# Kernel tuning notes

Hardware: AMD Instinct MI355X
Metric: run time of the kernel (lower is better)

## Reference

```python
import jax, jax.numpy as jnp
import numpy as np

EPS = 1e-6

def setup_inputs() -> dict:
    key = jax.random.key(0)
    ks = jax.random.split(key, 8)
    I, S, O = 1024, 512, 1024
    Bsz, T = 4, 2048
    return {
        "u": jax.random.normal(ks[0], (Bsz, T, I), dtype=jnp.float32),
        "dt": jax.random.normal(ks[1], (S,), dtype=jnp.float32),
        "A": jax.random.normal(ks[2], (S,), dtype=jnp.float32),
        "Bmat": jax.random.normal(ks[3], (I, S), dtype=jnp.float32) / np.sqrt(S),
        "C": jax.random.normal(ks[4], (S, O), dtype=jnp.float32) / np.sqrt(S),
        "D": jax.random.normal(ks[5], (O,), dtype=jnp.float32),
        "norm_w": jnp.ones((I,), dtype=jnp.float32),
    }

def _rmsnorm(x, w):
    x32 = x.astype(jnp.float32)
    n = x32 * jax.lax.rsqrt(jnp.mean(x32 * x32, axis=-1, keepdims=True) + EPS)
    return n.astype(x.dtype) * w

def reference(u, dt, A, Bmat, C, D, norm_w):
    u = _rmsnorm(u, norm_w)                      # [B, T, I]
    Bsz, T, _ = u.shape
    dts = jax.nn.sigmoid(dt)                     # [S]
    a = jnp.exp(-dts * jnp.abs(A))               # [S] discretized decay
    t = jnp.arange(T, dtype=jnp.float32)
    h = dts[:, None] * a[:, None] ** t[None, :]  # [S, T] geometric kernel
    u_proj = jnp.einsum('bti,is->bst', u, Bmat)  # [B, S, T]
    # depthwise causal conv: flipped kernel + cross-correlation == convolution
    k = jnp.flip(h, axis=1)[:, None, :]          # [S, 1, T] (OIW)
    x = jax.lax.conv_general_dilated(
        u_proj, k, window_strides=(1,), padding=[(T - 1, T - 1)],
        dimension_numbers=('NCW', 'OIW', 'NCW'),
        feature_group_count=u_proj.shape[1])[:, :, :T]  # [B, S, T]
    x = jnp.transpose(x, (0, 2, 1))              # [B, T, S]
    y = jnp.einsum('bts,so->bto', x, C) + D      # [B, T, O]
    return (y, x[:, -1])
```

## Files before the change

### kernel.cpp

```cpp
#include <hip/hip_runtime.h>
#include <math.h>

#define I_DIM 1024
#define S_DIM 512
#define O_DIM 1024
#define T_DIM 2048
#define B_SZ 4
#define M_ROWS (B_SZ * T_DIM)
#define EPSF 1e-6f

#define CL 64
#define NCH 32

typedef _Float16 f16;
typedef __attribute__((ext_vector_type(8))) _Float16 f16x8;
typedef __attribute__((ext_vector_type(2))) _Float16 f16x2;
typedef __attribute__((ext_vector_type(4))) float f32x4;

__device__ __forceinline__ unsigned short f2h_bits(float f) {
    _Float16 h = (_Float16)f;
    return __builtin_bit_cast(unsigned short, h);
}

__device__ __forceinline__ void load16_lds(const void* g, void* l) {
    __builtin_amdgcn_global_load_lds((const __attribute__((address_space(1))) void*)g,
                                     (__attribute__((address_space(3))) void*)l,
                                     16, 0, 0);
}

__global__ __launch_bounds__(256)
void prep_w(const float* __restrict__ Bmat, const float* __restrict__ dt,
            const float* __restrict__ nw, unsigned short* __restrict__ Bt16,
            const float* __restrict__ Cmat, unsigned short* __restrict__ Ct16) {
    __shared__ float tile[32][33];
    const int t = threadIdx.x;
    const int tx = t & 31, ty = t >> 5;
    const int bx = blockIdx.x;
    if (bx < 512) {
        const int bs = (bx & 15) * 32;
        const int bi = (bx >> 4) * 32;
        #pragma unroll
        for (int i = ty; i < 32; i += 8)
            tile[i][tx] = Bmat[(size_t)(bi + i) * S_DIM + bs + tx];
        __syncthreads();
        const float w = nw[bi + tx];
        #pragma unroll
        for (int i = ty; i < 32; i += 8) {
            const int s = bs + i;
            const float dts = 1.0f / (1.0f + expf(-dt[s]));
            Bt16[(size_t)s * I_DIM + bi + tx] = f2h_bits(tile[tx][i] * dts * w);
        }
    } else {
        const int tb = bx - 512;
        const int bo = (tb & 31) * 32;
        const int bs = (tb >> 5) * 32;
        #pragma unroll
        for (int i = ty; i < 32; i += 8)
            tile[i][tx] = Cmat[(size_t)(bs + i) * O_DIM + bo + tx];
        __syncthreads();
        #pragma unroll
        for (int i = ty; i < 32; i += 8)
            Ct16[(size_t)(bo + i) * S_DIM + bs + tx] = f2h_bits(tile[tx][i]);
    }
}

__global__ __launch_bounds__(256)
void gemm1_rms_chfin(const float* __restrict__ U, const f16* __restrict__ Bt,
                     f16* __restrict__ up, float* __restrict__ chlast,
                     const float* __restrict__ dt, const float* __restrict__ Avec) {
    constexpr int K = I_DIM, N = S_DIM, NK = K / 32;
    __shared__ f16 As[3][64 * 32];
    __shared__ f16 Bs[3][128 * 32];
    __shared__ float rsbuf[64];
    const int t = threadIdx.x;

    int bid = blockIdx.x;
    bid = (bid & 7) * 64 + (bid >> 3);
    const int n0 = (bid & 3) * 128;
    const int m0 = (bid >> 2) * 64;
    const int wid = t >> 6, lane = t & 63;
    const int wn = wid * 32, lr = lane & 15, kg = lane >> 4;

    const int swch = (t & 3) ^ ((t >> 3) & 3);
    const float* aptr = U + (size_t)(m0 + (t >> 2)) * K + swch * 8;
    const f16*  bptr = Bt + (size_t)(n0 + (t >> 2)) * K + swch * 8;
    const int rchunk = (kg ^ ((lr >> 1) & 3)) * 8;
    f16* adst = (f16*)&As[0][0] + t * 8;

    float ss = 0.f;
    f32x4 acc[4][2];
    #pragma unroll
    for (int i = 0; i < 4; ++i)
        #pragma unroll
        for (int j = 0; j < 2; ++j) acc[i][j] = (f32x4){0.f, 0.f, 0.f, 0.f};

    float4 rga[2], rgb[2];

    auto stageB = [&](int kt, int slot) {
        load16_lds(bptr + kt * 32, &Bs[slot][t * 8]);
        load16_lds(bptr + (size_t)64 * K + kt * 32, &Bs[slot][2048 + t * 8]);
    };
    auto writeA = [&](const float4* r, int slot) {
        ss += r[0].x * r[0].x + r[0].y * r[0].y + r[0].z * r[0].z + r[0].w * r[0].w
            + r[1].x * r[1].x + r[1].y * r[1].y + r[1].z * r[1].z + r[1].w * r[1].w;
        f16x8 h = { (_Float16)r[0].x, (_Float16)r[0].y, (_Float16)r[0].z, (_Float16)r[0].w,
                    (_Float16)r[1].x, (_Float16)r[1].y, (_Float16)r[1].z, (_Float16)r[1].w };
        *(f16x8*)(adst + slot * 2048) = h;
    };

    rga[0] = *(const float4*)(aptr);
    rga[1] = *(const float4*)(aptr + 4);
    stageB(0, 0);
    rgb[0] = *(const float4*)(aptr + 32);
    rgb[1] = *(const float4*)(aptr + 36);
    stageB(1, 1);
    asm volatile("s_waitcnt vmcnt(6)");
    writeA(rga, 0);

    #pragma unroll 2
    for (int kt = 0; kt < NK; ++kt) {
        asm volatile("s_waitcnt lgkmcnt(0)");
        if (kt + 1 < NK) asm volatile("s_waitcnt vmcnt(2)");
        else             asm volatile("s_waitcnt vmcnt(0)");
        __builtin_amdgcn_s_barrier();
        __builtin_amdgcn_sched_barrier(0);

        if (kt + 1 < NK)
            writeA(((kt + 1) & 1) ? rgb : rga, (kt + 1) % 3);
        if (kt + 2 < NK) {
            float4* r = (kt & 1) ? rgb : rga;
            const int k2 = (kt + 2) * 32;
            r[0] = *(const float4*)(aptr + k2);
            r[1] = *(const float4*)(aptr + k2 + 4);
            stageB(kt + 2, (kt + 2) % 3);
        }

        const int slot = kt % 3;
        f16x8 af[4], bf[2];
        #pragma unroll
        for (int m = 0; m < 4; ++m)
            af[m] = *(const f16x8*)&As[slot][(m * 16 + lr) * 32 + rchunk];
        #pragma unroll
        for (int n = 0; n < 2; ++n)
            bf[n] = *(const f16x8*)&Bs[slot][(wn + n * 16 + lr) * 32 + rchunk];
        #pragma unroll
        for (int m = 0; m < 4; ++m)
            #pragma unroll
            for (int n = 0; n < 2; ++n)
                acc[m][n] = __builtin_amdgcn_mfma_f32_16x16x32_f16(af[m], bf[n], acc[m][n], 0, 0, 0);
    }

    ss += __shfl_xor(ss, 1, 64);
    ss += __shfl_xor(ss, 2, 64);
    if ((t & 3) == 0) rsbuf[t >> 2] = rsqrtf(ss * (1.0f / K) + EPSF);
    __syncthreads();

    const int cb = m0 >> 11;
    const int cc = (m0 >> 6) & (NCH - 1);
    #pragma unroll
    for (int n = 0; n < 2; ++n) {
        const int col = n0 + wn + n * 16 + lr;
        const float dts = 1.0f / (1.0f + expf(-dt[col]));
        const float e = dts * fabsf(Avec[col]);
        const float ainv = expf(e);
        float partial = 0.f;
        #pragma unroll
        for (int m = 0; m < 4; ++m) {
            const int row = m * 16 + kg * 4;
            f32x4 rs4 = *(const f32x4*)&rsbuf[row];
            float wgt = expf(-e * (float)(63 - row));
            #pragma unroll
            for (int j = 0; j < 4; ++j) {
                const float val = rs4[j] * acc[m][n][j];
                up[(size_t)(m0 + row + j) * N + col] = (_Float16)val;
                partial = fmaf(wgt, val, partial);
                wgt *= ainv;
            }
        }
        partial += __shfl_xor(partial, 16, 64);
        partial += __shfl_xor(partial, 32, 64);
        if (kg == 0)
            chlast[(size_t)(cb * NCH + cc) * S_DIM + col] = partial;
    }
}

__global__ __launch_bounds__(256)
void gemm2_scan(const f16* __restrict__ upb, const float* __restrict__ chlast,
                const f16* __restrict__ Ct, const float* __restrict__ Dvec,
                const float* __restrict__ dt, const float* __restrict__ Avec,
                float* __restrict__ y, float* __restrict__ xlast) {
    constexpr int K = S_DIM, N = O_DIM, NK = K / 32;
    __shared__ __align__(16) unsigned char As[64 * 1024];
    __shared__ f16 Bs[2][128 * 32];
    const int t = threadIdx.x;

    int bid = blockIdx.x;
    bid = (bid & 7) * 128 + (bid >> 3);
    const int n0 = (bid & 7) * 128;
    const int m0 = (bid >> 3) * 64;
    const int wid = t >> 6, lane = t & 63;
    const int wn = wid * 32, lr = lane & 15, kg = lane >> 4;

    const int srcswz = ((t & 3) ^ ((t >> 3) & 3)) * 8;
    const f16* bptr = Ct + (size_t)(n0 + (t >> 2)) * K + srcswz;
    load16_lds(bptr, &Bs[0][t * 8]);
    load16_lds(bptr + (size_t)64 * K, &Bs[0][2048 + t * 8]);
    const int rchunk = (kg ^ ((lr >> 1) & 3)) * 8;

    const int cc = (m0 >> 6) & (NCH - 1);
    const int cb = m0 >> 11;
    const int s0 = 2 * t;
    const float dts0 = 1.0f / (1.0f + expf(-dt[s0]));
    const float dts1 = 1.0f / (1.0f + expf(-dt[s0 + 1]));
    const float ab0 = fabsf(Avec[s0]), ab1 = fabsf(Avec[s0 + 1]);
    const float g0 = expf(-dts0 * ab0);
    const float g1 = expf(-dts1 * ab1);
    const float gCL0 = expf(-dts0 * ab0 * (float)CL);
    const float gCL1 = expf(-dts1 * ab1 * (float)CL);
    const float2* ch = (const float2*)chlast;
    float cy0 = 0.f, cy1 = 0.f;
    {
        int j = 0;
        for (; j + 4 <= cc; j += 4) {
            float2 f0 = ch[(size_t)(cb * NCH + j + 0) * 256 + t];
            float2 f1 = ch[(size_t)(cb * NCH + j + 1) * 256 + t];
            float2 f2 = ch[(size_t)(cb * NCH + j + 2) * 256 + t];
            float2 f3 = ch[(size_t)(cb * NCH + j + 3) * 256 + t];
            cy0 = fmaf(gCL0, cy0, f0.x); cy1 = fmaf(gCL1, cy1, f0.y);
            cy0 = fmaf(gCL0, cy0, f1.x); cy1 = fmaf(gCL1, cy1, f1.y);
            cy0 = fmaf(gCL0, cy0, f2.x); cy1 = fmaf(gCL1, cy1, f2.y);
            cy0 = fmaf(gCL0, cy0, f3.x); cy1 = fmaf(gCL1, cy1, f3.y);
        }
        for (; j < cc; ++j) {
            float2 f = ch[(size_t)(cb * NCH + j) * 256 + t];
            cy0 = fmaf(gCL0, cy0, f.x);
            cy1 = fmaf(gCL1, cy1, f.y);
        }
    }

    const unsigned* up32 = (const unsigned*)upb;
    const size_t ub = (size_t)m0 * 256 + t;
    unsigned v[CL];
    #pragma unroll
    for (int j = 0; j < CL; ++j) v[j] = up32[ub + (size_t)j * 256];
    float x0 = cy0, x1 = cy1;
    #pragma unroll
    for (int j = 0; j < CL; ++j) {
        f16x2 h = __builtin_bit_cast(f16x2, v[j]);
        x0 = fmaf(g0, x0, (float)h.x);
        x1 = fmaf(g1, x1, (float)h.y);
        f16x2 o; o.x = (_Float16)x0; o.y = (_Float16)x1;
        v[j] = __builtin_bit_cast(unsigned, o);
    }
    #pragma unroll
    for (int j = 0; j < CL; ++j)
        *(unsigned*)&As[j * 1024 + ((t * 4) ^ ((j & 7) << 4))] = v[j];
    if (cc == NCH - 1)
        ((float2*)xlast)[cb * 256 + t] = make_float2(x0, x1);
    __syncthreads();

    f32x4 acc[4][2];
    #pragma unroll
    for (int i = 0; i < 4; ++i)
        #pragma unroll
        for (int j = 0; j < 2; ++j) acc[i][j] = (f32x4){0.f, 0.f, 0.f, 0.f};

    const int swz = (lr & 7) << 4;
    for (int kt = 0; kt < NK; ++kt) {
        const int cur = kt & 1;
        if (kt + 1 < NK) {
            const int k1 = (kt + 1) * 32;
            load16_lds(bptr + k1, &Bs[cur ^ 1][t * 8]);
            load16_lds(bptr + (size_t)64 * K + k1, &Bs[cur ^ 1][2048 + t * 8]);
            asm volatile("s_waitcnt vmcnt(2)");
        } else {
            asm volatile("s_waitcnt vmcnt(0)");
        }
        __builtin_amdgcn_s_barrier();
        __builtin_amdgcn_sched_barrier(0);

        f16x8 af[4], bf[2];
        #pragma unroll
        for (int m = 0; m < 4; ++m)
            af[m] = *(const f16x8*)&As[(m * 16 + lr) * 1024 + ((kt * 64 + kg * 16) ^ swz)];
        #pragma unroll
        for (int n = 0; n < 2; ++n)
            bf[n] = *(const f16x8*)&Bs[cur][(wn + n * 16 + lr) * 32 + rchunk];
        #pragma unroll
        for (int m = 0; m < 4; ++m)
            #pragma unroll
            for (int n = 0; n < 2; ++n)
                acc[m][n] = __builtin_amdgcn_mfma_f32_16x16x32_f16(af[m], bf[n], acc[m][n], 0, 0, 0);
        __builtin_amdgcn_s_barrier();
    }

    #pragma unroll
    for (int n = 0; n < 2; ++n) {
        const int col = n0 + wn + n * 16 + lr;
        const float dv = Dvec[col];
        #pragma unroll
        for (int m = 0; m < 4; ++m) {
            const int row = m0 + m * 16 + kg * 4;
            #pragma unroll
            for (int j = 0; j < 4; ++j)
                y[(size_t)(row + j) * N + col] = acc[m][n][j] + dv;
        }
    }
}

extern "C" void kernel_launch(void* const* d_in, const int* in_sizes, int n_in,
                              void* d_out, int out_size, void* d_ws, size_t ws_size,
                              hipStream_t stream) {
    const float* u    = (const float*)d_in[0];
    const float* dt   = (const float*)d_in[1];
    const float* Avec = (const float*)d_in[2];
    const float* Bmat = (const float*)d_in[3];
    const float* Cmat = (const float*)d_in[4];
    const float* Dvec = (const float*)d_in[5];
    const float* nw   = (const float*)d_in[6];

    float* y     = (float*)d_out;
    float* xlast = y + (size_t)M_ROWS * O_DIM;

    char* w = (char*)d_ws;
    f16*            up16   = (f16*)(w);
    unsigned short* Bt16   = (unsigned short*)(w + 8388608);
    unsigned short* Ct16   = (unsigned short*)(w + 9437184);
    float*          chlast = (float*)(w + 10485760);

    prep_w<<<1024, 256, 0, stream>>>(Bmat, dt, nw, Bt16, Cmat, Ct16);

    gemm1_rms_chfin<<<512, 256, 0, stream>>>(u, (const f16*)Bt16, up16, chlast, dt, Avec);

    gemm2_scan<<<1024, 256, 0, stream>>>(up16, chlast, (const f16*)Ct16, Dvec,
                                         dt, Avec, y, xlast);
}
```

Baseline: 56.49 us.

## Deepen software pipelines in both GEMMs and raise MFMA wave priority

In the first GEMM, A-tile global loads move from double to triple register buffering, prefetching three k-steps ahead, and the loop is fully unrolled with adjusted vmcnt waits. In the second GEMM, B staging goes to a triple-buffered LDS ring with two tiles in flight, which drops the trailing per-iteration barrier. Both MFMA blocks are wrapped in s_setprio so waves that are issuing matrix ops get priority. The aim is to hide global-load latency and cut barrier stalls, at the cost of more registers and LDS, which may lower occupancy.

Measured after the change: 65.43 us. 15.8% more time.

```diff
diff --git a/kernel.cpp b/kernel.cpp
--- a/kernel.cpp
+++ b/kernel.cpp
@@ -94,8 +94,13 @@
         #pragma unroll
         for (int j = 0; j < 2; ++j) acc[i][j] = (f32x4){0.f, 0.f, 0.f, 0.f};
 
-    float4 rga[2], rgb[2];
-
+    float4 Ar0[2], Ar1[2], Ar2[2];
+    auto aset = [&](int i) -> float4* { return i == 0 ? Ar0 : (i == 1 ? Ar1 : Ar2); };
+
+    auto loadA = [&](int kt, float4* r) {
+        r[0] = *(const float4*)(aptr + kt * 32);
+        r[1] = *(const float4*)(aptr + kt * 32 + 4);
+    };
     auto stageB = [&](int kt, int slot) {
         load16_lds(bptr + kt * 32, &Bs[slot][t * 8]);
         load16_lds(bptr + (size_t)64 * K + kt * 32, &Bs[slot][2048 + t * 8]);
@@ -108,32 +113,24 @@
         *(f16x8*)(adst + slot * 2048) = h;
     };
 
-    rga[0] = *(const float4*)(aptr);
-    rga[1] = *(const float4*)(aptr + 4);
-    stageB(0, 0);
-    rgb[0] = *(const float4*)(aptr + 32);
-    rgb[1] = *(const float4*)(aptr + 36);
-    stageB(1, 1);
-    asm volatile("s_waitcnt vmcnt(6)");
-    writeA(rga, 0);
-
-    #pragma unroll 2
+    loadA(0, Ar0); stageB(0, 0);
+    loadA(1, Ar1); stageB(1, 1);
+    loadA(2, Ar2);
+    asm volatile("s_waitcnt vmcnt(8)");
+    writeA(Ar0, 0);
+
+    #pragma unroll
     for (int kt = 0; kt < NK; ++kt) {
         asm volatile("s_waitcnt lgkmcnt(0)");
-        if (kt + 1 < NK) asm volatile("s_waitcnt vmcnt(2)");
-        else             asm volatile("s_waitcnt vmcnt(0)");
+        if (kt <= NK - 3)      asm volatile("s_waitcnt vmcnt(4)");
+        else if (kt == NK - 2) asm volatile("s_waitcnt vmcnt(2)");
+        else                   asm volatile("s_waitcnt vmcnt(0)");
         __builtin_amdgcn_s_barrier();
         __builtin_amdgcn_sched_barrier(0);
 
-        if (kt + 1 < NK)
-            writeA(((kt + 1) & 1) ? rgb : rga, (kt + 1) % 3);
-        if (kt + 2 < NK) {
-            float4* r = (kt & 1) ? rgb : rga;
-            const int k2 = (kt + 2) * 32;
-            r[0] = *(const float4*)(aptr + k2);
-            r[1] = *(const float4*)(aptr + k2 + 4);
-            stageB(kt + 2, (kt + 2) % 3);
-        }
+        if (kt + 1 < NK) writeA(aset((kt + 1) % 3), (kt + 1) % 3);
+        if (kt + 3 < NK) loadA(kt + 3, aset((kt + 3) % 3));
+        if (kt + 2 < NK) stageB(kt + 2, (kt + 2) % 3);
 
         const int slot = kt % 3;
         f16x8 af[4], bf[2];
@@ -143,11 +140,13 @@
         #pragma unroll
         for (int n = 0; n < 2; ++n)
             bf[n] = *(const f16x8*)&Bs[slot][(wn + n * 16 + lr) * 32 + rchunk];
+        __builtin_amdgcn_s_setprio(1);
         #pragma unroll
         for (int m = 0; m < 4; ++m)
             #pragma unroll
             for (int n = 0; n < 2; ++n)
                 acc[m][n] = __builtin_amdgcn_mfma_f32_16x16x32_f16(af[m], bf[n], acc[m][n], 0, 0, 0);
+        __builtin_amdgcn_s_setprio(0);
     }
 
     ss += __shfl_xor(ss, 1, 64);
@@ -191,7 +190,7 @@
                 float* __restrict__ y, float* __restrict__ xlast) {
     constexpr int K = S_DIM, N = O_DIM, NK = K / 32;
     __shared__ __align__(16) unsigned char As[64 * 1024];
-    __shared__ f16 Bs[2][128 * 32];
+    __shared__ f16 Bs[3][128 * 32];
     const int t = threadIdx.x;
 
     int bid = blockIdx.x;
@@ -203,8 +202,12 @@
 
     const int srcswz = ((t & 3) ^ ((t >> 3) & 3)) * 8;
     const f16* bptr = Ct + (size_t)(n0 + (t >> 2)) * K + srcswz;
-    load16_lds(bptr, &Bs[0][t * 8]);
-    load16_lds(bptr + (size_t)64 * K, &Bs[0][2048 + t * 8]);
+    auto stageB = [&](int kt, int slot) {
+        load16_lds(bptr + kt * 32, &Bs[slot][t * 8]);
+        load16_lds(bptr + (size_t)64 * K + kt * 32, &Bs[slot][2048 + t * 8]);
+    };
+    stageB(0, 0);
+    stageB(1, 1);
     const int rchunk = (kg ^ ((lr >> 1) & 3)) * 8;
 
     const int cc = (m0 >> 6) & (NCH - 1);
@@ -266,32 +269,31 @@
         for (int j = 0; j < 2; ++j) acc[i][j] = (f32x4){0.f, 0.f, 0.f, 0.f};
 
     const int swz = (lr & 7) << 4;
+    #pragma unroll
     for (int kt = 0; kt < NK; ++kt) {
-        const int cur = kt & 1;
-        if (kt + 1 < NK) {
-            const int k1 = (kt + 1) * 32;
-            load16_lds(bptr + k1, &Bs[cur ^ 1][t * 8]);
-            load16_lds(bptr + (size_t)64 * K + k1, &Bs[cur ^ 1][2048 + t * 8]);
-            asm volatile("s_waitcnt vmcnt(2)");
-        } else {
-            asm volatile("s_waitcnt vmcnt(0)");
-        }
-        __builtin_amdgcn_s_barrier();
-        __builtin_amdgcn_sched_barrier(0);
-
+        if (kt > 0) {
+            if (kt < NK - 1) asm volatile("s_waitcnt vmcnt(2)");
+            else             asm volatile("s_waitcnt vmcnt(0)");
+            __builtin_amdgcn_s_barrier();
+            __builtin_amdgcn_sched_barrier(0);
+        }
+        if (kt + 2 < NK) stageB(kt + 2, (kt + 2) % 3);
+
+        const int slot = kt % 3;
         f16x8 af[4], bf[2];
         #pragma unroll
         for (int m = 0; m < 4; ++m)
             af[m] = *(const f16x8*)&As[(m * 16 + lr) * 1024 + ((kt * 64 + kg * 16) ^ swz)];
         #pragma unroll
         for (int n = 0; n < 2; ++n)
-            bf[n] = *(const f16x8*)&Bs[cur][(wn + n * 16 + lr) * 32 + rchunk];
+            bf[n] = *(const f16x8*)&Bs[slot][(wn + n * 16 + lr) * 32 + rchunk];
+        __builtin_amdgcn_s_setprio(1);
         #pragma unroll
         for (int m = 0; m < 4; ++m)
             #pragma unroll
             for (int n = 0; n < 2; ++n)
                 acc[m][n] = __builtin_amdgcn_mfma_f32_16x16x32_f16(af[m], bf[n], acc[m][n], 0, 0, 0);
-        __builtin_amdgcn_s_barrier();
+        __builtin_amdgcn_s_setprio(0);
     }
 
     #pragma unroll
```
